# Kernel optimization log

Hardware: AMD Instinct MI355X
Metric: run time of the kernel (lower is better)

Reference implementation:

```python
import jax, jax.numpy as jnp
import numpy as np

LN2 = float(np.log(2.0))
CUTOFF_L = 0.5


def _ssp(x):
    # shifted softplus: log(0.5*exp(x) + 0.5)
    return jax.nn.softplus(x) - LN2


def _pair_idx(n):
    # ordered pairs arranged [n, n-1]: for each i, all j != i
    idx = np.arange(n)
    j = np.stack([np.concatenate([idx[:k], idx[k + 1:]]) for k in range(n)])  # [n, n-1]
    i = np.broadcast_to(idx[:, None], j.shape)
    return jnp.asarray(i), jnp.asarray(j)


def _mlp3(x, w1, b1, w2, b2, w3, b3):
    h = _ssp(x @ w1 + b1)
    h = _ssp(h @ w2 + b2)
    return h @ w3 + b3


def _backflow_cutoff(r, L=CUTOFF_L):
    r = r / L
    return jnp.where(r < L, r ** 2 * (6.0 - 8.0 * r + 3.0 * r ** 2), jnp.ones((), r.dtype))


def setup_inputs() -> dict:
    key = jax.random.key(0)
    ks = jax.random.split(key, 12)
    B, N, D, K = 512, 32, 256, 8
    dims_e = [D, 40, 6, 1]
    dims_n = [D, 81, 25, 8]

    def lin(k, fi, fo):
        return jax.random.normal(k, (fi, fo), jnp.float32) / np.sqrt(fi)

    inp = {
        'rs': jax.random.normal(ks[0], (B, N, 3), jnp.float32),
        'xs': jax.random.normal(ks[1], (B, N, D), jnp.float32),
        'coords': jax.random.normal(ks[2], (K, 3), jnp.float32) * 2.0,
        'ew1': lin(ks[3], dims_e[0], dims_e[1]), 'eb1': jnp.zeros((dims_e[1],), jnp.float32),
        'ew2': lin(ks[4], dims_e[1], dims_e[2]), 'eb2': jnp.zeros((dims_e[2],), jnp.float32),
        'ew3': lin(ks[5], dims_e[2], dims_e[3]), 'eb3': jnp.zeros((dims_e[3],), jnp.float32),
        'nw1': lin(ks[6], dims_n[0], dims_n[1]), 'nb1': jnp.zeros((dims_n[1],), jnp.float32),
        'nw2': lin(ks[7], dims_n[1], dims_n[2]), 'nb2': jnp.zeros((dims_n[2],), jnp.float32),
        'nw3': lin(ks[8], dims_n[2], dims_n[3]), 'nb3': jnp.zeros((dims_n[3],), jnp.float32),
    }
    return inp


def reference(rs, xs, coords, ew1, eb1, ew2, eb2, ew3, eb3,
              nw1, nb1, nw2, nb2, nw3, nb3):
    n_elec = rs.shape[-2]
    i, j = _pair_idx(n_elec)  # [n, n-1] static index arrays

    # electron-electron backflow
    diffs_elec = rs[..., i, :] - rs[..., j, :]                    # [B, n, n-1, 3]
    pair_feat = xs[..., i, :] * xs[..., j, :]                     # [B, n, n-1, D]
    w_pair = _mlp3(pair_feat, ew1, eb1, ew2, eb2, ew3, eb3)       # [B, n, n-1, 1]
    bf_elec = (w_pair * diffs_elec).sum(axis=-2)                  # [B, n, 3]

    # electron-nucleus backflow
    diffs_nuc = rs[..., :, None, :] - coords                      # [B, n, K, 3]
    w_nuc = _mlp3(xs, nw1, nb1, nw2, nb2, nw3, nb3)               # [B, n, K]
    bf_nuc = (w_nuc[..., None] * diffs_nuc).sum(axis=-2)          # [B, n, 3]

    dist_nuc = jnp.linalg.norm(diffs_nuc, axis=-1)                # [B, n, K]
    cutoff = _backflow_cutoff(dist_nuc).prod(axis=-1)             # [B, n]

    return rs + 1e-4 * cutoff[..., None] * (bf_elec + bf_nuc)
```

## Files before the change

kernel.cpp:

```cpp
#include <hip/hip_runtime.h>
#include <stdint.h>


static constexpr int B_ = 512, N_ = 32, D_ = 256, K_ = 8;
static constexpr int E1 = 40, E2 = 6;
static constexpr int N1 = 81, N2 = 25, N3 = 8;
static constexpr int HEP = 96;
static constexpr float LN2f = 0.69314718055994530942f;
static constexpr float L2Ef = 1.44269504088896340736f;

typedef float    f32x4 __attribute__((ext_vector_type(4)));
typedef _Float16 f16x8 __attribute__((ext_vector_type(8)));
typedef _Float16 f16x4 __attribute__((ext_vector_type(4)));

#define MFMA32(A, B, C) __builtin_amdgcn_mfma_f32_16x16x32_f16((A), (B), (C), 0, 0, 0)
#if __has_builtin(__builtin_amdgcn_mfma_f32_16x16x16_f16)
#define MFMA16(A, B, C) __builtin_amdgcn_mfma_f32_16x16x16_f16((A), (B), (C), 0, 0, 0)
#else
#define MFMA16(A, B, C) __builtin_amdgcn_mfma_f32_16x16x16f16((A), (B), (C), 0, 0, 0)
#endif

__device__ __forceinline__ float ssp2(float t) {
    float e = __builtin_amdgcn_exp2f(t);
    return __builtin_amdgcn_logf(fmaf(e, 0.5f, 0.5f));
}

__device__ __forceinline__ void lds_dma16(void* lds, const void* g) {
    __builtin_amdgcn_global_load_lds(
        (const __attribute__((address_space(1))) unsigned int*)(uintptr_t)g,
        (__attribute__((address_space(3))) unsigned int*)(uintptr_t)lds,
        16, 0, 0);
}

__global__ __launch_bounds__(256) void k_prep(
    const float* __restrict__ ew1, const float* __restrict__ nw1,
    const float* __restrict__ nw2, _Float16* __restrict__ wsp)
{
    const int g = blockIdx.x * 256 + threadIdx.x;
    _Float16* ew1T = wsp;
    _Float16* nw1T = wsp + 48 * 256;
    _Float16* nw2T = wsp + 48 * 256 + 96 * 256;

    if (g < 1536) {
        const int n = g >> 5, kb = g & 31;
        f16x8 v;
        #pragma unroll
        for (int d = 0; d < 8; ++d) {
            const int k = kb * 8 + d;
            v[d] = (_Float16)((n < E1) ? ew1[k * E1 + n] * L2Ef : 0.f);
        }
        *(f16x8*)&ew1T[n * 256 + ((kb ^ (n & 7)) << 3)] = v;
    } else if (g < 4608) {
        const int q = g - 1536;
        const int n = q >> 5, kb = q & 31;
        f16x8 v;
        #pragma unroll
        for (int d = 0; d < 8; ++d) {
            const int k = kb * 8 + d;
            v[d] = (_Float16)((n < N1) ? nw1[k * N1 + n] * L2Ef : 0.f);
        }
        *(f16x8*)&nw1T[n * 256 + kb * 8] = v;
    } else if (g < 4992) {
        const int q = g - 4608;
        const int n = q / 12, kb = q - n * 12;
        f16x8 v;
        #pragma unroll
        for (int d = 0; d < 8; ++d) {
            const int kk = kb * 8 + d;
            v[d] = (_Float16)((n < N2 && kk < N1) ? nw2[kk * N2 + n] : 0.f);
        }
        *(f16x8*)&nw2T[n * 96 + kb * 8] = v;
    }
}

__global__ __launch_bounds__(512, 3) void k_fused(
    const float* __restrict__ rs, const float* __restrict__ xs,
    const float* __restrict__ coords,
    const float* __restrict__ eb1, const float* __restrict__ ew2,
    const float* __restrict__ eb2, const float* __restrict__ ew3,
    const float* __restrict__ eb3, const float* __restrict__ nb1,
    const float* __restrict__ nb2, const float* __restrict__ nb3,
    const float* __restrict__ nw3, const _Float16* __restrict__ wsp,
    float* __restrict__ out)
{
    __shared__ alignas(16) _Float16 xs_h[N_ * 256];
    __shared__ alignas(16) _Float16 ew1T_s[48 * 256];
    __shared__ alignas(16) _Float16 h1e[16 * HEP];
    __shared__ alignas(16) float    h2e[16 * 26];
    __shared__ alignas(16) float    eb1_s[48];
    __shared__ alignas(16) float    b2_s[16];
    __shared__ float rs_s[96], nw3_s[200], nb2_s[32], nb3_s[8], co_s[24];
    __shared__ float bfn_s[48], cut_s[16], bfe_s[48];

    const int bid = blockIdx.x;
    const int b = bid >> 1, rbase = (bid & 1) << 4;
    const int t = threadIdx.x;
    const int wv = t >> 6, l = t & 63, quad = l >> 4, c = l & 15;

    const _Float16* ew1T_g = wsp;
    const _Float16* nw1T_g = wsp + 48 * 256;
    const _Float16* nw2T_g = wsp + 48 * 256 + 96 * 256;

    {
        const char* g = (const char*)ew1T_g;
        char* d = (char*)ew1T_s;
        const int wb = wv * 1024;
        #pragma unroll
        for (int r = 0; r < 3; ++r)
            lds_dma16(d + r * 8192 + wb, g + r * 8192 + wb + (l << 4));
    }
    {
        const float4* src = (const float4*)(xs + (size_t)b * N_ * D_);
        #pragma unroll
        for (int u = 0; u < 2; ++u) {
            const int idx = t + 512 * u;
            const int row = idx >> 5, kb = idx & 31;
            float4 v0 = src[idx << 1];
            float4 v1 = src[(idx << 1) + 1];
            union { _Float16 h[8]; uint4 q; } pk;
            pk.h[0] = (_Float16)v0.x; pk.h[1] = (_Float16)v0.y;
            pk.h[2] = (_Float16)v0.z; pk.h[3] = (_Float16)v0.w;
            pk.h[4] = (_Float16)v1.x; pk.h[5] = (_Float16)v1.y;
            pk.h[6] = (_Float16)v1.z; pk.h[7] = (_Float16)v1.w;
            *(uint4*)&xs_h[row * 256 + ((kb ^ (row & 7)) << 3)] = pk.q;
        }
    }
    if (t < 96)  rs_s[t] = rs[b * 96 + t];
    if (t < 200) nw3_s[t] = nw3[t] * LN2f;
    if (t < N2)  nb2_s[t] = nb2[t] * L2Ef;
    if (t < N3)  nb3_s[t] = nb3[t];
    if (t < 24)  co_s[t] = coords[t];
    if (t < 48)  eb1_s[t] = (t < E1) ? eb1[t] * L2Ef : 0.f;
    if (t < 16)  b2_s[t] = (t < E2) ? eb2[t] * L2Ef : 0.f;
    if (t < 384) ((uint64_t*)h1e)[t] = 0ull;

    f16x4 b2fT[3];
    #pragma unroll
    for (int Nt = 0; Nt < 3; ++Nt) {
        f16x4 p;
        #pragma unroll
        for (int r = 0; r < 4; ++r) {
            const int n = Nt * 16 + quad * 4 + r;
            p[r] = (_Float16)((n < E1 && c < E2) ? ew2[n * E2 + c] : 0.f);
        }
        b2fT[Nt] = p;
    }
    float w3q[4];
    #pragma unroll
    for (int r = 0; r < 4; ++r) {
        const int m = quad * 4 + r;
        w3q[r] = (m < E2) ? ew3[m] * LN2f : 0.f;
    }
    const float eb3v = eb3[0];

    __syncthreads();

    auto ee_round = [&](int lr) {
        const int i = rbase + lr;
        f32x4 acc[2][3];
        #pragma unroll
        for (int Nt = 0; Nt < 3; ++Nt) {
            f32x4 bias = *(const f32x4*)&eb1_s[Nt * 16 + quad * 4];
            acc[0][Nt] = bias;
            acc[1][Nt] = bias;
        }
        #pragma unroll
        for (int Kt = 0; Kt < 8; ++Kt) {
            const int kb = Kt * 4 + quad;
            const int sj = (kb ^ (c & 7)) << 3;
            f16x8 iv  = *(const f16x8*)&xs_h[i * 256 + ((kb ^ (i & 7)) << 3)];
            f16x8 jv0 = *(const f16x8*)&xs_h[c * 256 + sj];
            f16x8 jv1 = *(const f16x8*)&xs_h[(16 + c) * 256 + sj];
            f16x8 P0 = iv * jv0;
            f16x8 P1 = iv * jv1;
            #pragma unroll
            for (int Nt = 0; Nt < 3; ++Nt) {
                f16x8 b1 = *(const f16x8*)&ew1T_s[(Nt * 16 + c) * 256 + sj];
                acc[0][Nt] = MFMA32(b1, P0, acc[0][Nt]);
                acc[1][Nt] = MFMA32(b1, P1, acc[1][Nt]);
            }
        }
        const float rix = rs_s[i * 3 + 0], riy = rs_s[i * 3 + 1], riz = rs_s[i * 3 + 2];
        float cxi = 0.f, cyi = 0.f, czi = 0.f;
        const f32x4 b2i = *(const f32x4*)&b2_s[quad * 4];
        #pragma unroll
        for (int h = 0; h < 2; ++h) {
            f32x4 acc2 = b2i;
            #pragma unroll
            for (int Nt = 0; Nt < 3; ++Nt) {
                f16x4 bh_;
                #pragma unroll
                for (int r2 = 0; r2 < 4; ++r2)
                    bh_[r2] = (_Float16)ssp2(acc[h][Nt][r2]);
                acc2 = MFMA16(b2fT[Nt], bh_, acc2);
            }
            float wsum = 0.f;
            #pragma unroll
            for (int r2 = 0; r2 < 4; ++r2)
                wsum = fmaf(w3q[r2], ssp2(acc2[r2]), wsum);
            wsum += __shfl_xor(wsum, 16);
            wsum += __shfl_xor(wsum, 32);
            const float wj = wsum + eb3v;
            const int j = c + 16 * h;
            cxi = fmaf(wj, rix - rs_s[j * 3 + 0], cxi);
            cyi = fmaf(wj, riy - rs_s[j * 3 + 1], cyi);
            czi = fmaf(wj, riz - rs_s[j * 3 + 2], czi);
        }
        #pragma unroll
        for (int m2 = 1; m2 < 16; m2 <<= 1) {
            cxi += __shfl_xor(cxi, m2);
            cyi += __shfl_xor(cyi, m2);
            czi += __shfl_xor(czi, m2);
        }
        if (l == 0) {
            bfe_s[lr * 3 + 0] = cxi;
            bfe_s[lr * 3 + 1] = cyi;
            bfe_s[lr * 3 + 2] = czi;
        }
    };

    if (wv < 6) {
        const int n_col = wv * 16 + c;
        const float nb1v = (n_col < N1) ? nb1[n_col] * L2Ef : 0.f;
        const _Float16* bg = nw1T_g + n_col * 256 + quad * 8;
        f32x4 acc1 = (f32x4){0.f, 0.f, 0.f, 0.f};
        f16x8 Bp = *(const f16x8*)bg;
        #pragma unroll
        for (int Kt = 0; Kt < 8; ++Kt) {
            f16x8 Bf = Bp;
            if (Kt < 7) Bp = *(const f16x8*)(bg + (Kt + 1) * 32);
            f16x8 A = *(const f16x8*)&xs_h[(rbase + c) * 256 +
                                           (((Kt * 4 + quad) ^ (c & 7)) << 3)];
            acc1 = MFMA32(A, Bf, acc1);
        }
        if (n_col < N1) {
            #pragma unroll
            for (int r2 = 0; r2 < 4; ++r2)
                h1e[(quad * 4 + r2) * HEP + n_col] = (_Float16)ssp2(acc1[r2] + nb1v);
        }
    }
    ee_round(wv);
    __syncthreads();

    if (wv < 2) {
        const int n = wv * 16 + c;
        const _Float16* bg2 = nw2T_g + n * 96 + quad * 8;
        f32x4 acc2 = (f32x4){0.f, 0.f, 0.f, 0.f};
        #pragma unroll
        for (int Kt2 = 0; Kt2 < 3; ++Kt2) {
            f16x8 A  = *(const f16x8*)&h1e[c * HEP + Kt2 * 32 + quad * 8];
            f16x8 Bf = *(const f16x8*)(bg2 + Kt2 * 32);
            acc2 = MFMA32(A, Bf, acc2);
        }
        if (n < N2) {
            #pragma unroll
            for (int r2 = 0; r2 < 4; ++r2)
                h2e[(quad * 4 + r2) * 26 + n] = ssp2(acc2[r2] + nb2_s[n]);
        }
    }
    ee_round(wv + 8);
    __syncthreads();

    if (t < 128) {
        const int r = t >> 3, s = t & 7;
        const int gi = rbase + r;
        float w = nb3_s[s];
        const int rb26 = r * 26;
        #pragma unroll
        for (int kk = 0; kk < N2; ++kk)
            w = fmaf(h2e[rb26 + kk], nw3_s[kk * N3 + s], w);
        const float dx = rs_s[gi * 3 + 0] - co_s[s * 3 + 0];
        const float dy = rs_s[gi * 3 + 1] - co_s[s * 3 + 1];
        const float dz = rs_s[gi * 3 + 2] - co_s[s * 3 + 2];
        float cx = w * dx, cy = w * dy, cz = w * dz;
        #pragma unroll
        for (int m2 = 1; m2 < 8; m2 <<= 1) {
            cx += __shfl_xor(cx, m2);
            cy += __shfl_xor(cy, m2);
            cz += __shfl_xor(cz, m2);
        }
        const float rr  = sqrtf(dx * dx + dy * dy + dz * dz);
        const float xsc = 2.f * rr;
        float cf = (xsc < 0.5f) ? xsc * xsc * (6.f - 8.f * xsc + 3.f * xsc * xsc) : 1.f;
        #pragma unroll
        for (int m2 = 1; m2 < 8; m2 <<= 1) cf *= __shfl_xor(cf, m2);
        if (s == 0) {
            bfn_s[r * 3 + 0] = cx;
            bfn_s[r * 3 + 1] = cy;
            bfn_s[r * 3 + 2] = cz;
            cut_s[r] = cf;
        }
    }
    __syncthreads();

    if (t < 48) {
        const int r = t / 3;
        out[(size_t)b * (N_ * 3) + rbase * 3 + t] =
            rs_s[rbase * 3 + t] + 1e-4f * cut_s[r] * (bfe_s[t] + bfn_s[t]);
    }
}

extern "C" void kernel_launch(void* const* d_in, const int* in_sizes, int n_in,
                              void* d_out, int out_size, void* d_ws, size_t ws_size,
                              hipStream_t stream)
{
    const float* rs     = (const float*)d_in[0];
    const float* xs     = (const float*)d_in[1];
    const float* coords = (const float*)d_in[2];
    const float* ew1    = (const float*)d_in[3];
    const float* eb1    = (const float*)d_in[4];
    const float* ew2    = (const float*)d_in[5];
    const float* eb2    = (const float*)d_in[6];
    const float* ew3    = (const float*)d_in[7];
    const float* eb3    = (const float*)d_in[8];
    const float* nw1    = (const float*)d_in[9];
    const float* nb1    = (const float*)d_in[10];
    const float* nw2    = (const float*)d_in[11];
    const float* nb2    = (const float*)d_in[12];
    const float* nw3    = (const float*)d_in[13];
    const float* nb3    = (const float*)d_in[14];

    _Float16* wsp = (_Float16*)d_ws;

    k_prep<<<20, 256, 0, stream>>>(ew1, nw1, nw2, wsp);
    k_fused<<<B_ * 2, 512, 0, stream>>>(rs, xs, coords, eb1, ew2, eb2, ew3, eb3,
                                        nb1, nb2, nb3, nw3, wsp, (float*)d_out);
}
```

Measured before the change: 128.4 us.

## Process two electron rows per wave in one pass to reuse j and weight loads

The two separate ee_round calls, one before and one after the nucleus layer-2 stage, are merged into a single block. Each wave now computes rows i and i+8 together, so the xs_h j-rows and ew1T fragments are loaded once and feed four MFMA accumulator sets instead of two. This cuts LDS reads and lets more MFMAs be in flight per load. In exchange the accumulator register count doubles and launch bounds drop from 3 to 2 blocks per CU, so occupancy is lower and the ee work no longer overlaps the nucleus layer-2 stage.

```diff
diff --git a/kernel.cpp b/kernel.cpp
--- a/kernel.cpp
+++ b/kernel.cpp
@@ -73,7 +73,7 @@
     }
 }
 
-__global__ __launch_bounds__(512, 3) void k_fused(
+__global__ __launch_bounds__(512, 2) void k_fused(
     const float* __restrict__ rs, const float* __restrict__ xs,
     const float* __restrict__ coords,
     const float* __restrict__ eb1, const float* __restrict__ ew2,
@@ -155,70 +155,6 @@
 
     __syncthreads();
 
-    auto ee_round = [&](int lr) {
-        const int i = rbase + lr;
-        f32x4 acc[2][3];
-        #pragma unroll
-        for (int Nt = 0; Nt < 3; ++Nt) {
-            f32x4 bias = *(const f32x4*)&eb1_s[Nt * 16 + quad * 4];
-            acc[0][Nt] = bias;
-            acc[1][Nt] = bias;
-        }
-        #pragma unroll
-        for (int Kt = 0; Kt < 8; ++Kt) {
-            const int kb = Kt * 4 + quad;
-            const int sj = (kb ^ (c & 7)) << 3;
-            f16x8 iv  = *(const f16x8*)&xs_h[i * 256 + ((kb ^ (i & 7)) << 3)];
-            f16x8 jv0 = *(const f16x8*)&xs_h[c * 256 + sj];
-            f16x8 jv1 = *(const f16x8*)&xs_h[(16 + c) * 256 + sj];
-            f16x8 P0 = iv * jv0;
-            f16x8 P1 = iv * jv1;
-            #pragma unroll
-            for (int Nt = 0; Nt < 3; ++Nt) {
-                f16x8 b1 = *(const f16x8*)&ew1T_s[(Nt * 16 + c) * 256 + sj];
-                acc[0][Nt] = MFMA32(b1, P0, acc[0][Nt]);
-                acc[1][Nt] = MFMA32(b1, P1, acc[1][Nt]);
-            }
-        }
-        const float rix = rs_s[i * 3 + 0], riy = rs_s[i * 3 + 1], riz = rs_s[i * 3 + 2];
-        float cxi = 0.f, cyi = 0.f, czi = 0.f;
-        const f32x4 b2i = *(const f32x4*)&b2_s[quad * 4];
-        #pragma unroll
-        for (int h = 0; h < 2; ++h) {
-            f32x4 acc2 = b2i;
-            #pragma unroll
-            for (int Nt = 0; Nt < 3; ++Nt) {
-                f16x4 bh_;
-                #pragma unroll
-                for (int r2 = 0; r2 < 4; ++r2)
-                    bh_[r2] = (_Float16)ssp2(acc[h][Nt][r2]);
-                acc2 = MFMA16(b2fT[Nt], bh_, acc2);
-            }
-            float wsum = 0.f;
-            #pragma unroll
-            for (int r2 = 0; r2 < 4; ++r2)
-                wsum = fmaf(w3q[r2], ssp2(acc2[r2]), wsum);
-            wsum += __shfl_xor(wsum, 16);
-            wsum += __shfl_xor(wsum, 32);
-            const float wj = wsum + eb3v;
-            const int j = c + 16 * h;
-            cxi = fmaf(wj, rix - rs_s[j * 3 + 0], cxi);
-            cyi = fmaf(wj, riy - rs_s[j * 3 + 1], cyi);
-            czi = fmaf(wj, riz - rs_s[j * 3 + 2], czi);
-        }
-        #pragma unroll
-        for (int m2 = 1; m2 < 16; m2 <<= 1) {
-            cxi += __shfl_xor(cxi, m2);
-            cyi += __shfl_xor(cyi, m2);
-            czi += __shfl_xor(czi, m2);
-        }
-        if (l == 0) {
-            bfe_s[lr * 3 + 0] = cxi;
-            bfe_s[lr * 3 + 1] = cyi;
-            bfe_s[lr * 3 + 2] = czi;
-        }
-    };
-
     if (wv < 6) {
         const int n_col = wv * 16 + c;
         const float nb1v = (n_col < N1) ? nb1[n_col] * L2Ef : 0.f;
@@ -239,7 +175,81 @@
                 h1e[(quad * 4 + r2) * HEP + n_col] = (_Float16)ssp2(acc1[r2] + nb1v);
         }
     }
-    ee_round(wv);
+
+    {
+        const int i0 = rbase + wv, i1 = i0 + 8;
+        f32x4 acc[2][2][3];
+        #pragma unroll
+        for (int Nt = 0; Nt < 3; ++Nt) {
+            f32x4 bias = *(const f32x4*)&eb1_s[Nt * 16 + quad * 4];
+            acc[0][0][Nt] = bias; acc[0][1][Nt] = bias;
+            acc[1][0][Nt] = bias; acc[1][1][Nt] = bias;
+        }
+        #pragma unroll
+        for (int Kt = 0; Kt < 8; ++Kt) {
+            const int kb = Kt * 4 + quad;
+            const int sj = (kb ^ (c & 7)) << 3;
+            const int si = (kb ^ wv) << 3;
+            f16x8 iv0 = *(const f16x8*)&xs_h[i0 * 256 + si];
+            f16x8 iv1 = *(const f16x8*)&xs_h[i1 * 256 + si];
+            f16x8 jv0 = *(const f16x8*)&xs_h[c * 256 + sj];
+            f16x8 jv1 = *(const f16x8*)&xs_h[(16 + c) * 256 + sj];
+            f16x8 P00 = iv0 * jv0;
+            f16x8 P01 = iv0 * jv1;
+            f16x8 P10 = iv1 * jv0;
+            f16x8 P11 = iv1 * jv1;
+            #pragma unroll
+            for (int Nt = 0; Nt < 3; ++Nt) {
+                f16x8 b1 = *(const f16x8*)&ew1T_s[(Nt * 16 + c) * 256 + sj];
+                acc[0][0][Nt] = MFMA32(b1, P00, acc[0][0][Nt]);
+                acc[0][1][Nt] = MFMA32(b1, P01, acc[0][1][Nt]);
+                acc[1][0][Nt] = MFMA32(b1, P10, acc[1][0][Nt]);
+                acc[1][1][Nt] = MFMA32(b1, P11, acc[1][1][Nt]);
+            }
+        }
+        const f32x4 b2i = *(const f32x4*)&b2_s[quad * 4];
+        #pragma unroll
+        for (int ih = 0; ih < 2; ++ih) {
+            const int lr = wv + ih * 8, i = rbase + lr;
+            const float rix = rs_s[i * 3 + 0], riy = rs_s[i * 3 + 1],
+                        riz = rs_s[i * 3 + 2];
+            float cxi = 0.f, cyi = 0.f, czi = 0.f;
+            #pragma unroll
+            for (int h = 0; h < 2; ++h) {
+                f32x4 acc2 = b2i;
+                #pragma unroll
+                for (int Nt = 0; Nt < 3; ++Nt) {
+                    f16x4 bh_;
+                    #pragma unroll
+                    for (int r2 = 0; r2 < 4; ++r2)
+                        bh_[r2] = (_Float16)ssp2(acc[ih][h][Nt][r2]);
+                    acc2 = MFMA16(b2fT[Nt], bh_, acc2);
+                }
+                float wsum = 0.f;
+                #pragma unroll
+                for (int r2 = 0; r2 < 4; ++r2)
+                    wsum = fmaf(w3q[r2], ssp2(acc2[r2]), wsum);
+                wsum += __shfl_xor(wsum, 16);
+                wsum += __shfl_xor(wsum, 32);
+                const float wj = wsum + eb3v;
+                const int j = c + 16 * h;
+                cxi = fmaf(wj, rix - rs_s[j * 3 + 0], cxi);
+                cyi = fmaf(wj, riy - rs_s[j * 3 + 1], cyi);
+                czi = fmaf(wj, riz - rs_s[j * 3 + 2], czi);
+            }
+            #pragma unroll
+            for (int m2 = 1; m2 < 16; m2 <<= 1) {
+                cxi += __shfl_xor(cxi, m2);
+                cyi += __shfl_xor(cyi, m2);
+                czi += __shfl_xor(czi, m2);
+            }
+            if (l == 0) {
+                bfe_s[lr * 3 + 0] = cxi;
+                bfe_s[lr * 3 + 1] = cyi;
+                bfe_s[lr * 3 + 2] = czi;
+            }
+        }
+    }
     __syncthreads();
 
     if (wv < 2) {
@@ -258,7 +268,6 @@
                 h2e[(quad * 4 + r2) * 26 + n] = ssp2(acc2[r2] + nb2_s[n]);
         }
     }
-    ee_round(wv + 8);
     __syncthreads();
 
     if (t < 128) {
```

Result: faster. 124.5 us (-3.1%).
